# Performance work log

Measured on AMD Instinct MI355X. Metric: run time of the kernel, lower is better.

## Reference

```python
import jax, jax.numpy as jnp
import numpy as np

BANDWIDTH = 0.1
N_STEPS = 5
TOL = 1e-3
BASE = 3
COORD_OFFSET = 512   # bins assumed within (-512, 511] per dim
COORD_BITS = 10      # 3 dims * 10 bits = 30 bits, fits int32


def _generate_offsets(d, base=3):
    # replicates torch.meshgrid(indexing='ij') over arange(-1, base-1)
    ranges = [np.arange(-1, base - 1) for _ in range(d)]
    mesh = np.meshgrid(*ranges, indexing='ij')
    return jnp.asarray(np.stack(mesh, axis=-1).reshape(-1, d), dtype=jnp.int32)


def _pack_keys(bins):
    # bins: (..., d) int32 -> unique scalar int32 key per bin coordinate
    d = bins.shape[-1]
    key = jnp.zeros(bins.shape[:-1], dtype=jnp.int32)
    for k in range(d):  # tiny fixed loop over dims
        key = (key << COORD_BITS) | (bins[..., k] + COORD_OFFSET)
    return key


def _step(X, offsets, bandwidth):
    # One mean-shift step: bin points, scatter-add sums/counts over the
    # union of offset-shifted bins (torch.unique replaced by exact key
    # packing + sort-based grouping, fixed shapes for jit).
    n, d = X.shape
    m = offsets.shape[0]  # base ** d
    bins = (X / bandwidth).astype(jnp.int32)          # trunc-toward-zero == torch .int()
    shifted = bins[:, None, :] + offsets[None, :, :]  # (n, m, d)
    keys = _pack_keys(shifted).reshape(-1)            # (n*m,)
    K = keys.shape[0]

    order = jnp.argsort(keys)
    skeys = keys[order]
    new_grp = jnp.concatenate(
        [jnp.zeros((1,), jnp.int32), (skeys[1:] != skeys[:-1]).astype(jnp.int32)]
    )
    seg = jnp.cumsum(new_grp)                         # group id per sorted position

    # X repeated once per offset (matches X.repeat(1, m).reshape(-1, d))
    Xflat = jnp.broadcast_to(X[:, None, :], (n, m, d)).reshape(-1, d)
    sum_per = jax.ops.segment_sum(Xflat[order], seg, num_segments=K)          # (K, d)
    cnt_per = jax.ops.segment_sum(jnp.ones((K,), X.dtype), seg, num_segments=K)

    # segment id per original (unsorted) flat position == inverse_indices
    seg_orig = jnp.zeros((K,), seg.dtype).at[order].set(seg)
    sum_mapped = sum_per[seg_orig].reshape(n, m, d).sum(axis=1)   # (n, d)
    cnt_mapped = cnt_per[seg_orig].reshape(n, m).sum(axis=1)      # (n,)
    return sum_mapped / cnt_mapped[:, None]


def setup_inputs() -> dict:
    key = jax.random.key(0)
    X = jax.random.normal(key, (200000, 3), dtype=jnp.float32)
    return {"X": X}


def reference(X):
    n, d = X.shape
    offsets = _generate_offsets(d, BASE)

    def body(carry, _):
        Xc, done = carry
        Xn = _step(Xc, offsets, BANDWIDTH)
        Xn = jnp.where(done, Xc, Xn)  # freeze once converged (== early break)
        conv = jnp.max(jnp.linalg.norm(Xn - Xc, axis=1)) <= TOL
        return (Xn, done | conv), None

    (Xout, _), _ = jax.lax.scan(body, (X, jnp.array(False)), None, length=N_STEPS)
    return Xout
```

## Files before the change

### kernel.cpp

```cpp
#include <hip/hip_runtime.h>


constexpr float BW   = 0.1f;
constexpr float TOL2 = 1e-6f;
constexpr int DIM  = 112, OFF = 56;
constexpr int DIM2 = DIM * DIM;
constexpr int CELLS = DIM * DIM * DIM;
constexpr int CLW = CELLS / 32;
constexpr int RDIM = 16, RC = 7;
constexpr int NREG = RDIM * RDIM * RDIM;
constexpr int RC3 = RC * RC * RC;
constexpr int NB_A = 128, BLK = 256;
constexpr int NF = 2048;
constexpr int IPB = 51;
constexpr float FPS = 16777216.0f;
constexpr double FPSI = 1.0 / 16777216.0;

typedef float vf2 __attribute__((ext_vector_type(2)));

__device__ __forceinline__ int clampb(int v) { return v < 0 ? 0 : (v > DIM - 1 ? DIM - 1 : v); }
__device__ __forceinline__ int binf(float v) { return clampb((int)(v / BW) + OFF); }
__device__ __forceinline__ int flatb(int bx, int by, int bz) { return (bx * DIM + by) * DIM + bz; }
__device__ __forceinline__ int regOf(int bx, int by, int bz) {
    return ((bx / RC) * RDIM + (by / RC)) * RDIM + (bz / RC);
}
__device__ __forceinline__ int lcOf(int bx, int by, int bz) {
    return ((bx % RC) * RC + (by % RC)) * RC + (bz % RC);
}

__device__ __forceinline__ void pk_add(float* p, float a, float b) {
#if defined(__has_builtin) && __has_builtin(__builtin_amdgcn_global_atomic_fadd_v2f32)
    vf2 v = {a, b};
    __builtin_amdgcn_global_atomic_fadd_v2f32((vf2*)p, v);
#else
    atomicAdd(p, a);
    atomicAdd(p + 1, b);
#endif
}

__launch_bounds__(BLK)
__global__ void k_histA(const float* __restrict__ X, int n, int* __restrict__ blockHist,
                        float4* __restrict__ zeroB) {
    __shared__ int h[NREG];
    for (int i = threadIdx.x; i < NREG; i += blockDim.x) h[i] = 0;
    __syncthreads();
    int stride = gridDim.x * blockDim.x;
    for (int i = blockIdx.x * blockDim.x + threadIdx.x; i < n; i += stride) {
        float x = X[3 * i + 0], y = X[3 * i + 1], z = X[3 * i + 2];
        atomicAdd(&h[regOf(binf(x), binf(y), binf(z))], 1);
    }
    __syncthreads();
    for (int i = threadIdx.x; i < NREG; i += blockDim.x)
        blockHist[blockIdx.x * NREG + i] = h[i];
    for (int i = blockIdx.x * blockDim.x + threadIdx.x; i < CELLS; i += stride)
        zeroB[i] = make_float4(0.f, 0.f, 0.f, 0.f);
}

__global__ void k_colscan(int* __restrict__ blockHist, int* __restrict__ regionPS) {
    int r = blockIdx.x * blockDim.x + threadIdx.x;
    if (r >= NREG) return;
    int run = 0;
    for (int b = 0; b < NB_A; ++b) {
        int idx = b * NREG + r;
        int v = blockHist[idx];
        blockHist[idx] = run;
        run += v;
    }
    regionPS[r] = run;
}

__launch_bounds__(1024)
__global__ void k_regprefix(int* __restrict__ regionPS) {
    __shared__ int buf[1024];
    int t = threadIdx.x;
    int v0 = regionPS[4 * t + 0], v1 = regionPS[4 * t + 1];
    int v2 = regionPS[4 * t + 2], v3 = regionPS[4 * t + 3];
    int s = v0 + v1 + v2 + v3;
    buf[t] = s;
    __syncthreads();
    for (int d = 1; d < 1024; d <<= 1) {
        int add = (t >= d) ? buf[t - d] : 0;
        __syncthreads();
        buf[t] += add;
        __syncthreads();
    }
    int excl = buf[t] - s;
    regionPS[4 * t + 0] = excl;
    regionPS[4 * t + 1] = excl + v0;
    regionPS[4 * t + 2] = excl + v0 + v1;
    regionPS[4 * t + 3] = excl + v0 + v1 + v2;
    if (t == 1023) regionPS[4096] = buf[1023];
}

__launch_bounds__(BLK)
__global__ void k_scatterA(const float* __restrict__ X, int n,
                           const int* __restrict__ blockHist,
                           const int* __restrict__ regionPS,
                           float4* __restrict__ bucket) {
    __shared__ int cur[NREG];
    for (int i = threadIdx.x; i < NREG; i += blockDim.x) cur[i] = 0;
    __syncthreads();
    int stride = gridDim.x * blockDim.x;
    for (int i = blockIdx.x * blockDim.x + threadIdx.x; i < n; i += stride) {
        float x = X[3 * i + 0], y = X[3 * i + 1], z = X[3 * i + 2];
        int r = regOf(binf(x), binf(y), binf(z));
        int pos = regionPS[r] + blockHist[blockIdx.x * NREG + r] + atomicAdd(&cur[r], 1);
        bucket[pos] = make_float4(x, y, z, __int_as_float(i));
    }
}

__launch_bounds__(BLK)
__global__ void k_binB(const float4* __restrict__ bucket, const int* __restrict__ regionPS,
                       float4* __restrict__ A, int* __restrict__ E0,
                       int* __restrict__ PIdx, int* __restrict__ gM0) {
    __shared__ unsigned long long aX[RC3], aY[RC3], aZ[RC3];
    __shared__ unsigned aC[RC3];
    __shared__ int cidx[RC3];
    __shared__ int cnt, cur, sBase;
    int r = blockIdx.x;
    for (int c = threadIdx.x; c < RC3; c += blockDim.x) {
        aX[c] = 0ull; aY[c] = 0ull; aZ[c] = 0ull; aC[c] = 0u;
    }
    if (threadIdx.x == 0) { cnt = 0; cur = 0; }
    __syncthreads();
    int start = regionPS[r], end = regionPS[r + 1];
    for (int i = start + threadIdx.x; i < end; i += blockDim.x) {
        float4 p = bucket[i];
        int lc = lcOf(binf(p.x), binf(p.y), binf(p.z));
        atomicAdd(&aX[lc], (unsigned long long)(long long)rintf(p.x * FPS));
        atomicAdd(&aY[lc], (unsigned long long)(long long)rintf(p.y * FPS));
        atomicAdd(&aZ[lc], (unsigned long long)(long long)rintf(p.z * FPS));
        atomicAdd(&aC[lc], 1u);
    }
    __syncthreads();
    int myc = 0;
    for (int c = threadIdx.x; c < RC3; c += blockDim.x)
        if (aC[c] > 0u) ++myc;
    if (myc) atomicAdd(&cnt, myc);
    __syncthreads();
    if (threadIdx.x == 0 && cnt > 0) sBase = atomicAdd(gM0, cnt);
    __syncthreads();
    int rx = r / (RDIM * RDIM), ry = (r / RDIM) % RDIM, rz = r % RDIM;
    for (int c = threadIdx.x; c < RC3; c += blockDim.x) {
        if (aC[c] > 0u) {
            int idx = sBase + atomicAdd(&cur, 1);
            cidx[c] = idx;
            int bx = rx * RC + c / (RC * RC);
            int by = ry * RC + (c / RC) % RC;
            int bz = rz * RC + c % RC;
            int b = flatb(bx, by, bz);
            E0[idx] = b;
            A[b] = make_float4((float)((double)(long long)aX[c] * FPSI),
                               (float)((double)(long long)aY[c] * FPSI),
                               (float)((double)(long long)aZ[c] * FPSI),
                               (float)aC[c]);
        }
    }
    __syncthreads();
    for (int i = start + threadIdx.x; i < end; i += blockDim.x) {
        float4 p = bucket[i];
        int lc = lcOf(binf(p.x), binf(p.y), binf(p.z));
        PIdx[__float_as_int(p.w)] = cidx[lc];
    }
}

__launch_bounds__(BLK)
__global__ void k_fused(
    const float4* __restrict__ src, const int* __restrict__ list, const int* __restrict__ pK,
    float4* __restrict__ REo, int* __restrict__ IDXo, float4* __restrict__ eposInit,
    float4* __restrict__ tgt, unsigned* __restrict__ clT,
    int* __restrict__ listOut, int* __restrict__ pKout,
    int updS, const float* __restrict__ X, int n, const int* __restrict__ PIdx,
    const float4* __restrict__ REp, const int* __restrict__ IDXp,
    const int* __restrict__ pM0, float4* __restrict__ epos,
    unsigned* __restrict__ notConv,
    const int* __restrict__ clearList, const int* __restrict__ pKc,
    float4* __restrict__ clearGrid,
    unsigned* __restrict__ zeroMask, int zmW,
    float4* __restrict__ zeroGrid, int zgC, int lastStep) {
    __shared__ float4 sh[BLK];
    __shared__ unsigned sFlag;
    if (threadIdx.x == 0) sFlag = 0;
    __syncthreads();
    int K = *pK;
    int BC = (K + IPB - 1) / IPB;
    if (BC > NF - 256) BC = NF - 256;
    const float t5[5] = {1.f, 2.f, 3.f, 2.f, 1.f};
    int lane = threadIdx.x & 63;
    bool moved = false;

    if ((int)blockIdx.x < BC) {
        for (int ib = blockIdx.x; ib * IPB < K; ib += BC) {
            int li = threadIdx.x / 5;
            int dx = threadIdx.x % 5;
            int item = ib * IPB + li;
            float4 part = make_float4(0.f, 0.f, 0.f, 0.f);
            if (li < IPB && item < K) {
                int b = list[item];
                int bx = b / DIM2, rem = b % DIM2;
                int by = rem / DIM, bz = rem % DIM;
                int ix = bx + dx - 2;
                if ((unsigned)ix < (unsigned)DIM) {
                    float wx = t5[dx];
                    if (by >= 2 && by <= DIM - 3 && bz >= 2 && bz <= DIM - 3) {
                        #pragma unroll
                        for (int dy = 0; dy < 5; ++dy) {
                            float wxy = wx * t5[dy];
                            const float4* row = src + flatb(ix, by + dy - 2, bz - 2);
                            #pragma unroll
                            for (int dz = 0; dz < 5; ++dz) {
                                float w = wxy * t5[dz];
                                float4 e = row[dz];
                                part.x = fmaf(w, e.x, part.x);
                                part.y = fmaf(w, e.y, part.y);
                                part.z = fmaf(w, e.z, part.z);
                                part.w = fmaf(w, e.w, part.w);
                            }
                        }
                    } else {
                        for (int dy = 0; dy < 5; ++dy) {
                            int iy = by + dy - 2;
                            if ((unsigned)iy >= (unsigned)DIM) continue;
                            float wxy = wx * t5[dy];
                            for (int dz = 0; dz < 5; ++dz) {
                                int iz = bz + dz - 2;
                                if ((unsigned)iz >= (unsigned)DIM) continue;
                                float w = wxy * t5[dz];
                                float4 e = src[flatb(ix, iy, iz)];
                                part.x = fmaf(w, e.x, part.x);
                                part.y = fmaf(w, e.y, part.y);
                                part.z = fmaf(w, e.z, part.z);
                                part.w = fmaf(w, e.w, part.w);
                            }
                        }
                    }
                }
            }
            sh[threadIdx.x] = part;
            __syncthreads();
            if (threadIdx.x < IPB) {
                int item2 = ib * IPB + threadIdx.x;
                if (item2 < K) {
                    int base5 = threadIdx.x * 5;
                    float4 a0 = sh[base5 + 0], a1 = sh[base5 + 1], a2 = sh[base5 + 2];
                    float4 a3 = sh[base5 + 3], a4 = sh[base5 + 4];
                    float sx = a0.x + a1.x + a2.x + a3.x + a4.x;
                    float sy = a0.y + a1.y + a2.y + a3.y + a4.y;
                    float sz = a0.z + a1.z + a2.z + a3.z + a4.z;
                    float sc = a0.w + a1.w + a2.w + a3.w + a4.w;
                    int b = list[item2];
                    float W = src[b].w;
                    float4 np = make_float4(sx / sc, sy / sc, sz / sc, W);
                    REo[item2] = np;
                    IDXo[b] = item2;
                    if (eposInit) eposInit[item2] = np;
                    if (!lastStep) {
                        int bn = flatb(binf(np.x), binf(np.y), binf(np.z));
                        float* cell = (float*)&tgt[bn];
                        pk_add(cell + 0, W * np.x, W * np.y);
                        pk_add(cell + 2, W * np.z, W);
                        unsigned old = atomicOr(&clT[(unsigned)bn >> 5], 1u << (bn & 31));
                        bool isNew = !(old & (1u << (bn & 31)));
                        unsigned long long m = __ballot(isNew);
                        if (m) {
                            int leader = (int)__ffsll((long long)m) - 1;
                            int base;
                            if (lane == leader) base = atomicAdd(pKout, __popcll(m));
                            base = __shfl(base, leader, 64);
                            if (isNew) listOut[base + __popcll(m & ((1ull << lane) - 1))] = bn;
                        }
                    }
                }
            }
            __syncthreads();
        }
    } else {
        int U = (updS > 0) ? (X ? n : *pM0) : 0;
        int CL = clearList ? *pKc : 0;
        int total = U + CL + zmW + zgC;
        bool done = false;
        if (updS > 1) {
            for (int t = 1; t < updS; ++t) done |= (notConv[t] == 0u);
        }
        int stride = (NF - BC) * blockDim.x;
        for (int idx = (blockIdx.x - BC) * blockDim.x + threadIdx.x; idx < total;
             idx += stride) {
            if (idx < U) {
                int e = idx;
                if (X) {
                    float x = X[3 * e + 0], y = X[3 * e + 1], z = X[3 * e + 2];
                    float4 rr = REp[PIdx[e]];
                    float ex = rr.x - x, ey = rr.y - y, ez = rr.z - z;
                    moved |= (fmaf(ex, ex, fmaf(ey, ey, ez * ez)) > TOL2);
                } else if (!done) {
                    float4 p = epos[e];
                    int j = IDXp[flatb(binf(p.x), binf(p.y), binf(p.z))];
                    float4 rr = REp[j];
                    float ex = rr.x - p.x, ey = rr.y - p.y, ez = rr.z - p.z;
                    moved |= (fmaf(ex, ex, fmaf(ey, ey, ez * ez)) > TOL2);
                    epos[e] = make_float4(rr.x, rr.y, rr.z, p.w);
                }
            } else if (idx < U + CL) {
                clearGrid[clearList[idx - U]] = make_float4(0.f, 0.f, 0.f, 0.f);
            } else if (idx < U + CL + zmW) {
                zeroMask[idx - U - CL] = 0u;
            } else {
                zeroGrid[idx - U - CL - zmW] = make_float4(0.f, 0.f, 0.f, 0.f);
            }
        }
    }
    if (moved) sFlag = 1;
    __syncthreads();
    if (threadIdx.x == 0 && updS > 0 && sFlag) notConv[updS] = 1u;
}

__launch_bounds__(BLK)
__global__ void k_fin(const float4* __restrict__ REa, const int* __restrict__ IDXa,
                      const float4* __restrict__ epos, const int* __restrict__ pM0,
                      const unsigned* __restrict__ notConv, float4* __restrict__ fpos) {
    int M0 = *pM0;
    bool done = false;
    for (int t = 1; t <= 4; ++t) done |= (notConv[t] == 0u);
    for (int e = blockIdx.x * blockDim.x + threadIdx.x; e < M0;
         e += gridDim.x * blockDim.x) {
        float4 p = epos[e];
        if (!done) {
            float4 rr = REa[IDXa[flatb(binf(p.x), binf(p.y), binf(p.z))]];
            p.x = rr.x; p.y = rr.y; p.z = rr.z;
        }
        fpos[e] = p;
    }
}

__global__ void k_map(const int* __restrict__ PIdx, int n, const float4* __restrict__ fpos,
                      float* __restrict__ out) {
    int i = blockIdx.x * blockDim.x + threadIdx.x;
    if (i >= n) return;
    float4 p = fpos[PIdx[i]];
    out[3 * i + 0] = p.x;
    out[3 * i + 1] = p.y;
    out[3 * i + 2] = p.z;
}

extern "C" void kernel_launch(void* const* d_in, const int* in_sizes, int n_in,
                              void* d_out, int out_size, void* d_ws, size_t ws_size,
                              hipStream_t stream) {
    const float* X = (const float*)d_in[0];
    int n = in_sizes[0] / 3;

    char* ws = (char*)d_ws;
    int*      cnt     = (int*)ws;
    unsigned* notConv = (unsigned*)(ws + 32);
    size_t mB = (size_t)CLW * 4;
    size_t gB = (size_t)CELLS * 16;
    unsigned* m0 = (unsigned*)(ws + 256);
    unsigned* m1 = (unsigned*)(ws + 256 + mB);
    float4* A = (float4*)(ws + 256 + 2 * mB);
    float4* B = (float4*)((char*)A + gB);
    float4* C = (float4*)((char*)B + gB);
    int* IDXa = (int*)((char*)C + gB);
    int* IDXb = IDXa + CELLS;
    float4* REa  = (float4*)(IDXb + CELLS);
    float4* REb  = REa + n;
    float4* epos = REb + n;
    int* E0   = (int*)(epos + n);
    int* La   = E0 + n;
    int* Lb   = La + n;
    int* Lc   = Lb + n;
    int* PIdx = Lc + n;
    float4* bucket = (float4*)(PIdx + n);
    int* blockHist = (int*)(bucket + n);
    int* regionPS  = blockHist + NB_A * NREG;

    hipMemsetAsync(ws, 0, 256 + 2 * mB + gB, stream);

    k_histA<<<NB_A, BLK, 0, stream>>>(X, n, blockHist, B);
    k_colscan<<<NREG / BLK, BLK, 0, stream>>>(blockHist, regionPS);
    k_regprefix<<<1, 1024, 0, stream>>>(regionPS);
    k_scatterA<<<NB_A, BLK, 0, stream>>>(X, n, blockHist, regionPS, bucket);
    k_binB<<<NREG, BLK, 0, stream>>>(bucket, regionPS, A, E0, PIdx, &cnt[1]);

    k_fused<<<NF, BLK, 0, stream>>>(A, E0, &cnt[1], REa, IDXa, epos,
                                    B, m0, La, &cnt[2],
                                    0, nullptr, n, nullptr, nullptr, nullptr, nullptr,
                                    nullptr, notConv, nullptr, nullptr, nullptr,
                                    nullptr, 0, C, CELLS, 0);
    k_fused<<<NF, BLK, 0, stream>>>(B, La, &cnt[2], REb, IDXb, nullptr,
                                    C, m1, Lb, &cnt[3],
                                    1, X, n, PIdx, REa, IDXa, &cnt[1], nullptr,
                                    notConv, E0, &cnt[1], A,
                                    m0, CLW, nullptr, 0, 0);
    k_fused<<<NF, BLK, 0, stream>>>(C, Lb, &cnt[3], REa, IDXa, nullptr,
                                    A, m0, Lc, &cnt[4],
                                    2, nullptr, n, nullptr, REb, IDXb, &cnt[1], epos,
                                    notConv, La, &cnt[2], B,
                                    m1, CLW, nullptr, 0, 0);
    k_fused<<<NF, BLK, 0, stream>>>(A, Lc, &cnt[4], REb, IDXb, nullptr,
                                    B, m1, La, &cnt[5],
                                    3, nullptr, n, nullptr, REa, IDXa, &cnt[1], epos,
                                    notConv, nullptr, nullptr, nullptr,
                                    nullptr, 0, nullptr, 0, 0);
    k_fused<<<NF, BLK, 0, stream>>>(B, La, &cnt[5], REa, IDXa, nullptr,
                                    nullptr, nullptr, nullptr, nullptr,
                                    4, nullptr, n, nullptr, REb, IDXb, &cnt[1], epos,
                                    notConv, nullptr, nullptr, nullptr,
                                    nullptr, 0, nullptr, 0, 1);

    k_fin<<<256, BLK, 0, stream>>>(REa, IDXa, epos, &cnt[1], notConv, REb);
    k_map<<<(n + BLK - 1) / BLK, BLK, 0, stream>>>(PIdx, n, REb, (float*)d_out);
}
```

Measured before the change: 284.9 us.

## Build occupied-cell lists via separate bitmask compaction kernel instead of atomic append

```diff
diff --git a/kernel.cpp b/kernel.cpp
--- a/kernel.cpp
+++ b/kernel.cpp
@@ -96,7 +96,7 @@
 __global__ void k_scatterA(const float* __restrict__ X, int n,
                            const int* __restrict__ blockHist,
                            const int* __restrict__ regionPS,
-                           float4* __restrict__ bucket) {
+                           float4* __restrict__ bucket, float4* __restrict__ zeroC) {
     __shared__ int cur[NREG];
     for (int i = threadIdx.x; i < NREG; i += blockDim.x) cur[i] = 0;
     __syncthreads();
@@ -107,6 +107,8 @@
         int pos = regionPS[r] + blockHist[blockIdx.x * NREG + r] + atomicAdd(&cur[r], 1);
         bucket[pos] = make_float4(x, y, z, __int_as_float(i));
     }
+    for (int i = blockIdx.x * blockDim.x + threadIdx.x; i < CELLS; i += stride)
+        zeroC[i] = make_float4(0.f, 0.f, 0.f, 0.f);
 }
 
 __launch_bounds__(BLK)
@@ -165,19 +167,47 @@
 }
 
 __launch_bounds__(BLK)
+__global__ void k_compactM(unsigned* __restrict__ mask, int* __restrict__ listOut,
+                           int* __restrict__ pKout) {
+    __shared__ int scan[BLK];
+    __shared__ int sBase;
+    int i = blockIdx.x * blockDim.x + threadIdx.x;
+    unsigned w = (i < CLW) ? mask[i] : 0u;
+    if (i < CLW && w) mask[i] = 0u;
+    int c = __popc(w);
+    scan[threadIdx.x] = c;
+    __syncthreads();
+    for (int d = 1; d < BLK; d <<= 1) {
+        int add = (threadIdx.x >= (unsigned)d) ? scan[threadIdx.x - d] : 0;
+        __syncthreads();
+        scan[threadIdx.x] += add;
+        __syncthreads();
+    }
+    if (threadIdx.x == BLK - 1) {
+        int tot = scan[BLK - 1];
+        sBase = tot ? atomicAdd(pKout, tot) : 0;
+    }
+    __syncthreads();
+    int base = sBase + scan[threadIdx.x] - c;
+    int bb = i * 32;
+    while (w) {
+        int b = __ffs(w) - 1;
+        listOut[base++] = bb + b;
+        w &= w - 1;
+    }
+}
+
+__launch_bounds__(BLK)
 __global__ void k_fused(
     const float4* __restrict__ src, const int* __restrict__ list, const int* __restrict__ pK,
     float4* __restrict__ REo, int* __restrict__ IDXo, float4* __restrict__ eposInit,
     float4* __restrict__ tgt, unsigned* __restrict__ clT,
-    int* __restrict__ listOut, int* __restrict__ pKout,
     int updS, const float* __restrict__ X, int n, const int* __restrict__ PIdx,
     const float4* __restrict__ REp, const int* __restrict__ IDXp,
     const int* __restrict__ pM0, float4* __restrict__ epos,
     unsigned* __restrict__ notConv,
     const int* __restrict__ clearList, const int* __restrict__ pKc,
-    float4* __restrict__ clearGrid,
-    unsigned* __restrict__ zeroMask, int zmW,
-    float4* __restrict__ zeroGrid, int zgC, int lastStep) {
+    float4* __restrict__ clearGrid, int lastStep) {
     __shared__ float4 sh[BLK];
     __shared__ unsigned sFlag;
     if (threadIdx.x == 0) sFlag = 0;
@@ -186,7 +216,6 @@
     int BC = (K + IPB - 1) / IPB;
     if (BC > NF - 256) BC = NF - 256;
     const float t5[5] = {1.f, 2.f, 3.f, 2.f, 1.f};
-    int lane = threadIdx.x & 63;
     bool moved = false;
 
     if ((int)blockIdx.x < BC) {
@@ -259,16 +288,7 @@
                         float* cell = (float*)&tgt[bn];
                         pk_add(cell + 0, W * np.x, W * np.y);
                         pk_add(cell + 2, W * np.z, W);
-                        unsigned old = atomicOr(&clT[(unsigned)bn >> 5], 1u << (bn & 31));
-                        bool isNew = !(old & (1u << (bn & 31)));
-                        unsigned long long m = __ballot(isNew);
-                        if (m) {
-                            int leader = (int)__ffsll((long long)m) - 1;
-                            int base;
-                            if (lane == leader) base = atomicAdd(pKout, __popcll(m));
-                            base = __shfl(base, leader, 64);
-                            if (isNew) listOut[base + __popcll(m & ((1ull << lane) - 1))] = bn;
-                        }
+                        atomicOr(&clT[(unsigned)bn >> 5], 1u << (bn & 31));
                     }
                 }
             }
@@ -277,7 +297,7 @@
     } else {
         int U = (updS > 0) ? (X ? n : *pM0) : 0;
         int CL = clearList ? *pKc : 0;
-        int total = U + CL + zmW + zgC;
+        int total = U + CL;
         bool done = false;
         if (updS > 1) {
             for (int t = 1; t < updS; ++t) done |= (notConv[t] == 0u);
@@ -300,12 +320,8 @@
                     moved |= (fmaf(ex, ex, fmaf(ey, ey, ez * ez)) > TOL2);
                     epos[e] = make_float4(rr.x, rr.y, rr.z, p.w);
                 }
-            } else if (idx < U + CL) {
+            } else {
                 clearGrid[clearList[idx - U]] = make_float4(0.f, 0.f, 0.f, 0.f);
-            } else if (idx < U + CL + zmW) {
-                zeroMask[idx - U - CL] = 0u;
-            } else {
-                zeroGrid[idx - U - CL - zmW] = make_float4(0.f, 0.f, 0.f, 0.f);
             }
         }
     }
@@ -367,44 +383,46 @@
     int* La   = E0 + n;
     int* Lb   = La + n;
     int* Lc   = Lb + n;
-    int* PIdx = Lc + n;
+    int* Ld   = Lc + n;
+    int* PIdx = Ld + n;
     float4* bucket = (float4*)(PIdx + n);
     int* blockHist = (int*)(bucket + n);
     int* regionPS  = blockHist + NB_A * NREG;
 
     hipMemsetAsync(ws, 0, 256 + 2 * mB + gB, stream);
 
+    const int NCM = (CLW + BLK - 1) / BLK;
+
     k_histA<<<NB_A, BLK, 0, stream>>>(X, n, blockHist, B);
     k_colscan<<<NREG / BLK, BLK, 0, stream>>>(blockHist, regionPS);
     k_regprefix<<<1, 1024, 0, stream>>>(regionPS);
-    k_scatterA<<<NB_A, BLK, 0, stream>>>(X, n, blockHist, regionPS, bucket);
+    k_scatterA<<<NB_A, BLK, 0, stream>>>(X, n, blockHist, regionPS, bucket, C);
     k_binB<<<NREG, BLK, 0, stream>>>(bucket, regionPS, A, E0, PIdx, &cnt[1]);
 
     k_fused<<<NF, BLK, 0, stream>>>(A, E0, &cnt[1], REa, IDXa, epos,
-                                    B, m0, La, &cnt[2],
+                                    B, m0,
                                     0, nullptr, n, nullptr, nullptr, nullptr, nullptr,
-                                    nullptr, notConv, nullptr, nullptr, nullptr,
-                                    nullptr, 0, C, CELLS, 0);
+                                    nullptr, notConv, nullptr, nullptr, nullptr, 0);
+    k_compactM<<<NCM, BLK, 0, stream>>>(m0, La, &cnt[2]);
     k_fused<<<NF, BLK, 0, stream>>>(B, La, &cnt[2], REb, IDXb, nullptr,
-                                    C, m1, Lb, &cnt[3],
+                                    C, m1,
                                     1, X, n, PIdx, REa, IDXa, &cnt[1], nullptr,
-                                    notConv, E0, &cnt[1], A,
-                                    m0, CLW, nullptr, 0, 0);
+                                    notConv, E0, &cnt[1], A, 0);
+    k_compactM<<<NCM, BLK, 0, stream>>>(m1, Lb, &cnt[3]);
     k_fused<<<NF, BLK, 0, stream>>>(C, Lb, &cnt[3], REa, IDXa, nullptr,
-                                    A, m0, Lc, &cnt[4],
+                                    A, m0,
                                     2, nullptr, n, nullptr, REb, IDXb, &cnt[1], epos,
-                                    notConv, La, &cnt[2], B,
-                                    m1, CLW, nullptr, 0, 0);
+                                    notConv, La, &cnt[2], B, 0);
+    k_compactM<<<NCM, BLK, 0, stream>>>(m0, Lc, &cnt[4]);
     k_fused<<<NF, BLK, 0, stream>>>(A, Lc, &cnt[4], REb, IDXb, nullptr,
-                                    B, m1, La, &cnt[5],
+                                    B, m1,
                                     3, nullptr, n, nullptr, REa, IDXa, &cnt[1], epos,
-                                    notConv, nullptr, nullptr, nullptr,
-                                    nullptr, 0, nullptr, 0, 0);
-    k_fused<<<NF, BLK, 0, stream>>>(B, La, &cnt[5], REa, IDXa, nullptr,
-                                    nullptr, nullptr, nullptr, nullptr,
+                                    notConv, nullptr, nullptr, nullptr, 0);
+    k_compactM<<<NCM, BLK, 0, stream>>>(m1, Ld, &cnt[5]);
+    k_fused<<<NF, BLK, 0, stream>>>(B, Ld, &cnt[5], REa, IDXa, nullptr,
+                                    nullptr, nullptr,
                                     4, nullptr, n, nullptr, REb, IDXb, &cnt[1], epos,
-                                    notConv, nullptr, nullptr, nullptr,
-                                    nullptr, 0, nullptr, 0, 1);
+                                    notConv, nullptr, nullptr, nullptr, 1);
 
     k_fin<<<256, BLK, 0, stream>>>(REa, IDXa, epos, &cnt[1], notConv, REb);
     k_map<<<(n + BLK - 1) / BLK, BLK, 0, stream>>>(PIdx, n, REb, (float*)d_out);
```

Result: faster. 253.0 us (-11.2%).
